# Kernel optimization log

Hardware: AMD Instinct MI355X
Metric: run time of the kernel (lower is better)

Reference implementation:

```python
import jax, jax.numpy as jnp
import numpy as np

STATE_DIM, ACTION_DIM, HIDDEN_DIM = 512, 64, 2048
INPUT_DIM = STATE_DIM + ACTION_DIM + 1  # 577
BATCH = 4096


def setup_inputs() -> dict:
    key = jax.random.key(0)
    ks = jax.random.split(key, 12)
    sc_x = 1.0 / np.sqrt(INPUT_DIM)
    sc_h = 1.0 / np.sqrt(HIDDEN_DIM)
    return {
        "s": jax.random.normal(ks[0], (BATCH, STATE_DIM), jnp.float32),
        "a_prev": jax.random.normal(ks[1], (BATCH, ACTION_DIM), jnp.float32),
        "r_prev": jax.random.normal(ks[2], (BATCH, 1), jnp.float32),
        "h": jnp.zeros((HIDDEN_DIM,), jnp.float32),
        "c": jnp.zeros((HIDDEN_DIM,), jnp.float32),
        # Fused gate weights: columns ordered [i, f, g(c-tilde), o]
        "Wx": jax.random.uniform(ks[3], (INPUT_DIM, 4 * HIDDEN_DIM), jnp.float32, -sc_x, sc_x),
        "Wh": jax.random.uniform(ks[4], (HIDDEN_DIM, 4 * HIDDEN_DIM), jnp.float32, -sc_h, sc_h),
        "bh": jax.random.uniform(ks[5], (4 * HIDDEN_DIM,), jnp.float32, -sc_h, sc_h),
        "Wa": jax.random.uniform(ks[6], (HIDDEN_DIM, ACTION_DIM), jnp.float32, -sc_h, sc_h),
        "ba": jax.random.uniform(ks[7], (ACTION_DIM,), jnp.float32, -sc_h, sc_h),
        "Wv": jax.random.uniform(ks[8], (HIDDEN_DIM, 1), jnp.float32, -sc_h, sc_h),
        "bv": jax.random.uniform(ks[9], (1,), jnp.float32, -sc_h, sc_h),
    }


def reference(s, a_prev, r_prev, h, c, Wx, Wh, bh, Wa, ba, Wv, bv):
    # x: [B, input_dim]
    x = jnp.concatenate([s, a_prev, r_prev], axis=1)
    # Two fused GEMMs replace the 8 separate small linears (same math).
    z = x @ Wx + h @ Wh + bh          # [B, 4H]
    zi, zf, zg, zo = jnp.split(z, 4, axis=-1)
    i = jax.nn.sigmoid(zi)
    f = jax.nn.sigmoid(zf)
    c_new = f * c + i * jnp.tanh(zg)  # [B, H] (c broadcast over batch)
    o = jax.nn.sigmoid(zo)
    h_new = o * jnp.tanh(c_new)       # [B, H]
    probs = jax.nn.softmax(h_new @ Wa + ba, axis=1)  # [B, A]
    v = h_new @ Wv + bv               # [B, 1]
    return (probs, v)
```

## Files before the change

kernel.cpp:

```cpp
#include <hip/hip_runtime.h>
#include <hip/hip_bf16.h>

#define BATCH   4096
#define SDIM    512
#define ADIM    64
#define IDIM    577
#define KP2     640
#define NKT64   10
#define HDIM    2048
#define ZDIM    8192
#define BUFE    (128 * 64)

typedef __attribute__((ext_vector_type(8))) __bf16 bf16x8;
typedef __attribute__((ext_vector_type(4))) float  accx4;

__global__ __launch_bounds__(256) void setup_kernel(
    const float* __restrict__ s, const float* __restrict__ a_prev,
    const float* __restrict__ r_prev, const float* __restrict__ h,
    const float* __restrict__ wx, const float* __restrict__ wh,
    const float* __restrict__ wa,
    __hip_bfloat16* __restrict__ xb, __hip_bfloat16* __restrict__ wxt,
    __hip_bfloat16* __restrict__ waT, float* __restrict__ zh_w)
{
    __shared__ float stile[64 * 65];
    const int bid = blockIdx.x;
    const int t = threadIdx.x;

    if (bid < 1280) {
        const int kt2 = bid >> 7;
        const int nt  = bid & 127;
        const int c4  = t & 15;
        const int rr  = t >> 4;
#pragma unroll
        for (int i = 0; i < 4; ++i) {
            const int r = rr + i * 16;
            const int k = kt2 * 64 + r;
            float4 v = (k < IDIM)
                ? *(const float4*)(wx + (size_t)k * ZDIM + nt * 64 + c4 * 4)
                : float4{0.f, 0.f, 0.f, 0.f};
            *(float4*)(stile + r * 65 + c4 * 4) = v;
        }
        __syncthreads();
        const int ch = t & 7;
#pragma unroll
        for (int i = 0; i < 2; ++i) {
            const int nr = (t >> 3) + i * 32;
            bf16x8 w8;
#pragma unroll
            for (int j = 0; j < 8; ++j)
                w8[j] = (__bf16)stile[(ch * 8 + j) * 65 + nr];
            *(bf16x8*)(wxt + (size_t)(nt * 64 + nr) * KP2 + kt2 * 64 + ch * 8)
                = w8;
        }
    } else if (bid < 1536) {
        const int zb = bid - 1280;
        const int nb = zb & 31, ky = zb >> 5;
        const int n  = nb * 256 + t;
        const float* hp  = h + ky * 256;
        const float* whp = wh + (size_t)ky * 256 * ZDIM + n;
        float p = 0.0f;
#pragma unroll 16
        for (int kk = 0; kk < 256; ++kk)
            p = fmaf(hp[kk], whp[(size_t)kk * ZDIM], p);
        zh_w[ky * ZDIM + n] = p;
    } else if (bid < 5632) {
        const int row = bid - 1536;
        const float* srow = s + (size_t)row * SDIM;
        const float* arow = a_prev + (size_t)row * ADIM;
        __hip_bfloat16* xrow = xb + (size_t)row * KP2;
        for (int c = t; c < KP2; c += 256) {
            float v;
            if (c < SDIM)        v = srow[c];
            else if (c < 576)    v = arow[c - SDIM];
            else if (c == 576)   v = r_prev[row];
            else                 v = 0.0f;
            xrow[c] = __float2bfloat16(v);
        }
    } else {
        const int wb = bid - 5632;
        const int kt = wb >> 1, at = wb & 1;
        const int c  = t & 31, r0 = t >> 5;
#pragma unroll
        for (int i = 0; i < 4; ++i) {
            int r = r0 + i * 8;
            stile[r * 33 + c] = wa[(size_t)(kt * 32 + r) * ADIM + at * 32 + c];
        }
        __syncthreads();
#pragma unroll
        for (int i = 0; i < 4; ++i) {
            int r = r0 + i * 8;
            waT[(size_t)(at * 32 + r) * HDIM + kt * 32 + c] =
                __float2bfloat16(stile[c * 33 + r]);
        }
    }
}

__global__ __launch_bounds__(256) void zh_reduce(
    const float* __restrict__ zh_w, const float* __restrict__ bh,
    float* __restrict__ zh)
{
    const int j = blockIdx.x * 256 + threadIdx.x;
    float v = bh[j];
#pragma unroll
    for (int p = 0; p < 8; ++p)
        v += zh_w[p * ZDIM + j];
    zh[j] = v;
}

__device__ __forceinline__ float sigmoid_f(float x) {
    return 1.0f / (1.0f + __expf(-x));
}
__device__ __forceinline__ float tanh_f(float x) {
    return 1.0f - 2.0f / (1.0f + __expf(2.0f * x));
}

__global__ __launch_bounds__(256, 2) void lstm_gemm(
    const __hip_bfloat16* __restrict__ xb,
    const __hip_bfloat16* __restrict__ wxt,
    const float* __restrict__ zh,
    const float* __restrict__ cvec,
    __hip_bfloat16* __restrict__ hout)
{
    __shared__ __bf16 smA[2 * BUFE];
    __shared__ __bf16 smB[2 * BUFE];
    const int t    = threadIdx.x;
    const int lane = t & 63;
    const int wid  = t >> 6;
    const int m0   = blockIdx.x * 128;
    const int n0   = blockIdx.y * 32;
    const int wm   = wid >> 1, wn = wid & 1;
    const int fl15 = lane & 15;
    const int fhi  = lane >> 4;

    accx4 acc[4][4] = {};

    const int srow = lane >> 3;
    const int slot = lane & 7;
    const int cch  = slot ^ srow;
    const __bf16* gA[4]; const __bf16* gB[4]; int lofs[4];
#pragma unroll
    for (int i = 0; i < 4; ++i) {
        const int r = wid * 32 + i * 8 + srow;
        gA[i] = (const __bf16*)xb + (size_t)(m0 + r) * KP2 + cch * 8;
        const int g = r >> 5, nn = r & 31;
        gB[i] = (const __bf16*)wxt +
                (size_t)(g * HDIM + n0 + nn) * KP2 + cch * 8;
        lofs[i] = (wid * 32 + i * 8) * 64;
    }

    auto stage = [&](int tile, int p) {
        const int ko = tile * 64;
        const int po = p * BUFE;
#pragma unroll
        for (int i = 0; i < 4; ++i) {
            __builtin_amdgcn_global_load_lds(
                (const __attribute__((address_space(1))) void*)(gA[i] + ko),
                (__attribute__((address_space(3))) void*)(smA + po + lofs[i]),
                16, 0, 0);
            __builtin_amdgcn_global_load_lds(
                (const __attribute__((address_space(1))) void*)(gB[i] + ko),
                (__attribute__((address_space(3))) void*)(smB + po + lofs[i]),
                16, 0, 0);
        }
    };

    auto compute = [&](int p) {
        const int po = p * BUFE;
#pragma unroll
        for (int hf = 0; hf < 2; ++hf) {
            const int ck = hf * 4 + fhi;
            const int sl = (ck ^ (fl15 & 7)) * 8;
            bf16x8 af[4], bfr[4];
#pragma unroll
            for (int rt = 0; rt < 4; ++rt)
                af[rt] = *(const bf16x8*)(smA + po +
                    (wm * 64 + rt * 16 + fl15) * 64 + sl);
#pragma unroll
            for (int g = 0; g < 4; ++g)
                bfr[g] = *(const bf16x8*)(smB + po +
                    (g * 32 + wn * 16 + fl15) * 64 + sl);
#pragma unroll
            for (int g = 0; g < 4; ++g)
#pragma unroll
                for (int rt = 0; rt < 4; ++rt)
                    acc[g][rt] = __builtin_amdgcn_mfma_f32_16x16x32_bf16(
                        af[rt], bfr[g], acc[g][rt], 0, 0, 0);
        }
    };

    stage(0, 0);
    __syncthreads();
#pragma unroll
    for (int kt = 0; kt < NKT64 - 1; ++kt) {
        stage(kt + 1, (kt + 1) & 1);
        compute(kt & 1);
        __syncthreads();
    }
    compute((NKT64 - 1) & 1);

    const int colg = n0 + wn * 16 + fl15;
    const float zhi = zh[colg];
    const float zhf = zh[HDIM + colg];
    const float zhg = zh[2 * HDIM + colg];
    const float zho = zh[3 * HDIM + colg];
    const float cv  = cvec[colg];
#pragma unroll
    for (int rt = 0; rt < 4; ++rt) {
#pragma unroll
        for (int r = 0; r < 4; ++r) {
            const int row = m0 + wm * 64 + rt * 16 + (fhi << 2) + r;
            const float zi = acc[0][rt][r] + zhi;
            const float zf = acc[1][rt][r] + zhf;
            const float zg = acc[2][rt][r] + zhg;
            const float zo = acc[3][rt][r] + zho;
            const float cn = sigmoid_f(zf) * cv + sigmoid_f(zi) * tanh_f(zg);
            const float hn = sigmoid_f(zo) * tanh_f(cn);
            hout[(size_t)row * HDIM + colg] = __float2bfloat16(hn);
        }
    }
}

__global__ __launch_bounds__(512) void head_kernel(
    const __hip_bfloat16* __restrict__ hnew,
    const __hip_bfloat16* __restrict__ waT,
    const float* __restrict__ wv,
    const float* __restrict__ ba, const float* __restrict__ bv,
    float* __restrict__ probs, float* __restrict__ vout)
{
    __shared__ float lg[8][16][68];
    __shared__ float vpart[8][16];
    const int t    = threadIdx.x;
    const int lane = t & 63;
    const int w    = t >> 6;
    const int r0   = blockIdx.x * 16;
    const int fl15 = lane & 15, fhi = lane >> 4;
    const int k0   = w * 256;

    const __bf16* arow = (const __bf16*)hnew +
        (size_t)(r0 + fl15) * HDIM + k0 + fhi * 8;
    const __bf16* brow = (const __bf16*)waT +
        (size_t)fl15 * HDIM + k0 + fhi * 8;
    const float* wvp = wv + k0 + fhi * 8;

    accx4 acc[4] = {};
    float va0 = 0.f, va1 = 0.f;
#pragma unroll
    for (int kk = 0; kk < 256; kk += 32) {
        bf16x8 af = *(const bf16x8*)(arow + kk);
#pragma unroll
        for (int a = 0; a < 4; ++a) {
            bf16x8 bf = *(const bf16x8*)(brow + (size_t)a * 16 * HDIM + kk);
            acc[a] = __builtin_amdgcn_mfma_f32_16x16x32_bf16(
                af, bf, acc[a], 0, 0, 0);
        }
#pragma unroll
        for (int j = 0; j < 4; ++j) {
            va0 = fmaf((float)af[j],     wvp[kk + j],     va0);
            va1 = fmaf((float)af[j + 4], wvp[kk + j + 4], va1);
        }
    }
#pragma unroll
    for (int a = 0; a < 4; ++a)
#pragma unroll
        for (int r = 0; r < 4; ++r)
            lg[w][fhi * 4 + r][a * 16 + fl15] = acc[a][r];
    float va = va0 + va1;
    va += __shfl_xor(va, 16);
    va += __shfl_xor(va, 32);
    if (lane < 16) vpart[w][lane] = va;
    __syncthreads();

    const float bav = ba[lane];
#pragma unroll
    for (int i = 0; i < 2; ++i) {
        const int row = w * 2 + i;
        float logit = bav;
#pragma unroll
        for (int p = 0; p < 8; ++p)
            logit += lg[p][row][lane];
        float m = logit;
#pragma unroll
        for (int mask = 32; mask >= 1; mask >>= 1)
            m = fmaxf(m, __shfl_xor(m, mask));
        const float e = __expf(logit - m);
        float ssum = e;
#pragma unroll
        for (int mask = 32; mask >= 1; mask >>= 1)
            ssum += __shfl_xor(ssum, mask);
        probs[(size_t)(r0 + row) * 64 + lane] = e / ssum;
    }
    if (t < 16) {
        float v = bv[0];
#pragma unroll
        for (int p = 0; p < 8; ++p)
            v += vpart[p][t];
        vout[r0 + t] = v;
    }
}

extern "C" void kernel_launch(void* const* d_in, const int* in_sizes, int n_in,
                              void* d_out, int out_size, void* d_ws,
                              size_t ws_size, hipStream_t stream)
{
    const float* s      = (const float*)d_in[0];
    const float* a_prev = (const float*)d_in[1];
    const float* r_prev = (const float*)d_in[2];
    const float* h      = (const float*)d_in[3];
    const float* c      = (const float*)d_in[4];
    const float* Wx     = (const float*)d_in[5];
    const float* Wh     = (const float*)d_in[6];
    const float* bh     = (const float*)d_in[7];
    const float* Wa     = (const float*)d_in[8];
    const float* ba     = (const float*)d_in[9];
    const float* Wv     = (const float*)d_in[10];
    const float* bv     = (const float*)d_in[11];

    float* out   = (float*)d_out;
    float* probs = out;
    float* vout  = out + (size_t)BATCH * ADIM;

    char* ws = (char*)d_ws;
    __hip_bfloat16* xb   = (__hip_bfloat16*)ws;
    __hip_bfloat16* wxt  = (__hip_bfloat16*)(ws + 5242880);
    __hip_bfloat16* waT  = (__hip_bfloat16*)(ws + 15728640);
    float* zh_w          = (float*)(ws + 15990784);
    float* zh            = (float*)(ws + 16252928);
    __hip_bfloat16* hnew = (__hip_bfloat16*)(ws + 16285696);

    setup_kernel<<<5760, 256, 0, stream>>>(
        s, a_prev, r_prev, h, Wx, Wh, Wa, xb, wxt, waT, zh_w);
    zh_reduce<<<ZDIM / 256, 256, 0, stream>>>(zh_w, bh, zh);
    lstm_gemm<<<dim3(BATCH / 128, HDIM / 32), 256, 0, stream>>>(
        xb, wxt, zh, c, hnew);
    head_kernel<<<BATCH / 16, 512, 0, stream>>>(
        hnew, waT, Wv, ba, bv, probs, vout);
}
```

Baseline: 213.2 us.

## Load B fragments directly to registers and fuse zh reduction into GEMM epilogue

```diff
diff --git a/kernel.cpp b/kernel.cpp
--- a/kernel.cpp
+++ b/kernel.cpp
@@ -95,18 +95,6 @@
     }
 }
 
-__global__ __launch_bounds__(256) void zh_reduce(
-    const float* __restrict__ zh_w, const float* __restrict__ bh,
-    float* __restrict__ zh)
-{
-    const int j = blockIdx.x * 256 + threadIdx.x;
-    float v = bh[j];
-#pragma unroll
-    for (int p = 0; p < 8; ++p)
-        v += zh_w[p * ZDIM + j];
-    zh[j] = v;
-}
-
 __device__ __forceinline__ float sigmoid_f(float x) {
     return 1.0f / (1.0f + __expf(-x));
 }
@@ -117,12 +105,12 @@
 __global__ __launch_bounds__(256, 2) void lstm_gemm(
     const __hip_bfloat16* __restrict__ xb,
     const __hip_bfloat16* __restrict__ wxt,
-    const float* __restrict__ zh,
+    const float* __restrict__ zh_w,
+    const float* __restrict__ bh,
     const float* __restrict__ cvec,
     __hip_bfloat16* __restrict__ hout)
 {
     __shared__ __bf16 smA[2 * BUFE];
-    __shared__ __bf16 smB[2 * BUFE];
     const int t    = threadIdx.x;
     const int lane = t & 63;
     const int wid  = t >> 6;
@@ -137,82 +125,97 @@
     const int srow = lane >> 3;
     const int slot = lane & 7;
     const int cch  = slot ^ srow;
-    const __bf16* gA[4]; const __bf16* gB[4]; int lofs[4];
+    const __bf16* gA[4]; int lofs[4];
 #pragma unroll
     for (int i = 0; i < 4; ++i) {
         const int r = wid * 32 + i * 8 + srow;
         gA[i] = (const __bf16*)xb + (size_t)(m0 + r) * KP2 + cch * 8;
-        const int g = r >> 5, nn = r & 31;
-        gB[i] = (const __bf16*)wxt +
-                (size_t)(g * HDIM + n0 + nn) * KP2 + cch * 8;
         lofs[i] = (wid * 32 + i * 8) * 64;
     }
 
-    auto stage = [&](int tile, int p) {
+    const __bf16* gB[4];
+#pragma unroll
+    for (int g = 0; g < 4; ++g)
+        gB[g] = (const __bf16*)wxt +
+            (size_t)(g * HDIM + n0 + wn * 16 + fl15) * KP2 + fhi * 8;
+
+    auto stageA = [&](int tile, int p) {
         const int ko = tile * 64;
         const int po = p * BUFE;
 #pragma unroll
-        for (int i = 0; i < 4; ++i) {
+        for (int i = 0; i < 4; ++i)
             __builtin_amdgcn_global_load_lds(
                 (const __attribute__((address_space(1))) void*)(gA[i] + ko),
                 (__attribute__((address_space(3))) void*)(smA + po + lofs[i]),
                 16, 0, 0);
-            __builtin_amdgcn_global_load_lds(
-                (const __attribute__((address_space(1))) void*)(gB[i] + ko),
-                (__attribute__((address_space(3))) void*)(smB + po + lofs[i]),
-                16, 0, 0);
-        }
     };
 
-    auto compute = [&](int p) {
-        const int po = p * BUFE;
+    bf16x8 bcur[4][2], bnext[4][2];
+    auto loadB = [&](int tile, bf16x8 (&b)[4][2]) {
+        const int ko = tile * 64;
+#pragma unroll
+        for (int g = 0; g < 4; ++g)
+#pragma unroll
+            for (int hf = 0; hf < 2; ++hf)
+                b[g][hf] = *(const bf16x8*)(gB[g] + ko + hf * 32);
+    };
+
+    stageA(0, 0);
+    loadB(0, bcur);
+    __syncthreads();
+
+#pragma unroll
+    for (int kt = 0; kt < NKT64; ++kt) {
+        if (kt < NKT64 - 1) {
+            stageA(kt + 1, (kt + 1) & 1);
+            loadB(kt + 1, bnext);
+        }
+        const int po = (kt & 1) * BUFE;
 #pragma unroll
         for (int hf = 0; hf < 2; ++hf) {
-            const int ck = hf * 4 + fhi;
-            const int sl = (ck ^ (fl15 & 7)) * 8;
-            bf16x8 af[4], bfr[4];
+            const int sl = ((hf * 4 + fhi) ^ (fl15 & 7)) * 8;
+            bf16x8 af[4];
 #pragma unroll
             for (int rt = 0; rt < 4; ++rt)
                 af[rt] = *(const bf16x8*)(smA + po +
                     (wm * 64 + rt * 16 + fl15) * 64 + sl);
 #pragma unroll
             for (int g = 0; g < 4; ++g)
-                bfr[g] = *(const bf16x8*)(smB + po +
-                    (g * 32 + wn * 16 + fl15) * 64 + sl);
-#pragma unroll
-            for (int g = 0; g < 4; ++g)
 #pragma unroll
                 for (int rt = 0; rt < 4; ++rt)
                     acc[g][rt] = __builtin_amdgcn_mfma_f32_16x16x32_bf16(
-                        af[rt], bfr[g], acc[g][rt], 0, 0, 0);
-        }
-    };
-
-    stage(0, 0);
-    __syncthreads();
-#pragma unroll
-    for (int kt = 0; kt < NKT64 - 1; ++kt) {
-        stage(kt + 1, (kt + 1) & 1);
-        compute(kt & 1);
-        __syncthreads();
-    }
-    compute((NKT64 - 1) & 1);
+                        af[rt], bcur[g][hf], acc[g][rt], 0, 0, 0);
+        }
+        if (kt < NKT64 - 1) {
+            __syncthreads();
+#pragma unroll
+            for (int g = 0; g < 4; ++g)
+#pragma unroll
+                for (int hf = 0; hf < 2; ++hf)
+                    bcur[g][hf] = bnext[g][hf];
+        }
+    }
 
     const int colg = n0 + wn * 16 + fl15;
-    const float zhi = zh[colg];
-    const float zhf = zh[HDIM + colg];
-    const float zhg = zh[2 * HDIM + colg];
-    const float zho = zh[3 * HDIM + colg];
-    const float cv  = cvec[colg];
+    float zsum[4];
+#pragma unroll
+    for (int g = 0; g < 4; ++g) {
+        float z = bh[g * HDIM + colg];
+#pragma unroll
+        for (int j = 0; j < 8; ++j)
+            z += zh_w[j * ZDIM + g * HDIM + colg];
+        zsum[g] = z;
+    }
+    const float cv = cvec[colg];
 #pragma unroll
     for (int rt = 0; rt < 4; ++rt) {
 #pragma unroll
         for (int r = 0; r < 4; ++r) {
             const int row = m0 + wm * 64 + rt * 16 + (fhi << 2) + r;
-            const float zi = acc[0][rt][r] + zhi;
-            const float zf = acc[1][rt][r] + zhf;
-            const float zg = acc[2][rt][r] + zhg;
-            const float zo = acc[3][rt][r] + zho;
+            const float zi = acc[0][rt][r] + zsum[0];
+            const float zf = acc[1][rt][r] + zsum[1];
+            const float zg = acc[2][rt][r] + zsum[2];
+            const float zo = acc[3][rt][r] + zsum[3];
             const float cn = sigmoid_f(zf) * cv + sigmoid_f(zi) * tanh_f(zg);
             const float hn = sigmoid_f(zo) * tanh_f(cn);
             hout[(size_t)row * HDIM + colg] = __float2bfloat16(hn);
@@ -324,14 +327,12 @@
     __hip_bfloat16* wxt  = (__hip_bfloat16*)(ws + 5242880);
     __hip_bfloat16* waT  = (__hip_bfloat16*)(ws + 15728640);
     float* zh_w          = (float*)(ws + 15990784);
-    float* zh            = (float*)(ws + 16252928);
-    __hip_bfloat16* hnew = (__hip_bfloat16*)(ws + 16285696);
+    __hip_bfloat16* hnew = (__hip_bfloat16*)(ws + 16252928);
 
     setup_kernel<<<5760, 256, 0, stream>>>(
         s, a_prev, r_prev, h, Wx, Wh, Wa, xb, wxt, waT, zh_w);
-    zh_reduce<<<ZDIM / 256, 256, 0, stream>>>(zh_w, bh, zh);
     lstm_gemm<<<dim3(BATCH / 128, HDIM / 32), 256, 0, stream>>>(
-        xb, wxt, zh, c, hnew);
+        xb, wxt, zh_w, bh, c, hnew);
     head_kernel<<<BATCH / 16, 512, 0, stream>>>(
         hnew, waT, Wv, ba, bv, probs, vout);
 }
```

Measured after the change: 242.5 us. +13.7%, slower.
